# Kernel optimization log

Hardware: AMD Instinct MI355X
Metric: run time of the kernel (lower is better)

## Reference

```python
import jax, jax.numpy as jnp
import numpy as np

B, C_IN, C_MID, C_OUT, R, K = 2048, 64, 64, 128, 60, 13
EPS = 1e-5


def _gather(x, nei):
    # x: [B, C, 60] -> gather neighbors -> [B, C, 60, 13]
    b, c = x.shape[0], x.shape[1]
    return x[:, :, nei].reshape(b, c, R, K)


def _block(x, nei, g, bta, m, v, W, c):
    # BN (eval mode) -> ReLU -> Conv2d(kernel (1,13)) fused block.
    h = _gather(x, nei)                              # [B,C,60,13]
    inv = g * jax.lax.rsqrt(v + EPS)                 # [C]
    h = jax.nn.relu(h * inv[None, :, None, None] + (bta - m * inv)[None, :, None, None])
    # Conv2d with kernel (1,13), stride 1 == contraction over (c, k)
    return jnp.einsum('bcrk,ock->bor', h, W) + c[None, :, None]  # [B,O,60]


def setup_inputs() -> dict:
    key = jax.random.key(0)
    ks = jax.random.split(key, 24)
    n = lambda k, s: jax.random.normal(k, s, dtype=jnp.float32)
    u = lambda k, s: jax.random.uniform(k, s, dtype=jnp.float32, minval=0.5, maxval=1.5)
    return {
        "x": n(ks[0], (B, C_IN, R)),
        "nei": jax.random.randint(ks[1], (R * K,), 0, R, dtype=jnp.int32),
        # comb_layer_in: BN(in) + Conv(in->mid)
        "g1": n(ks[2], (C_IN,)), "b1": n(ks[3], (C_IN,)), "m1": n(ks[4], (C_IN,)), "v1": u(ks[5], (C_IN,)),
        "W1": n(ks[6], (C_MID, C_IN, K)) * 0.1, "c1": n(ks[7], (C_MID,)) * 0.1,
        # comb_layer_out: BN(mid) + Conv(mid->out)
        "g2": n(ks[8], (C_MID,)), "b2": n(ks[9], (C_MID,)), "m2": n(ks[10], (C_MID,)), "v2": u(ks[11], (C_MID,)),
        "W2": n(ks[12], (C_OUT, C_MID, K)) * 0.1, "c2": n(ks[13], (C_OUT,)) * 0.1,
        # short_cut_layer: BN(in) + Conv(in->out)
        "g3": n(ks[14], (C_IN,)), "b3": n(ks[15], (C_IN,)), "m3": n(ks[16], (C_IN,)), "v3": u(ks[17], (C_IN,)),
        "W3": n(ks[18], (C_OUT, C_IN, K)) * 0.1, "c3": n(ks[19], (C_OUT,)) * 0.1,
    }


def reference(x, nei, g1, b1, m1, v1, W1, c1, g2, b2, m2, v2, W2, c2,
              g3, b3, m3, v3, W3, c3):
    f = _block(x, nei, g1, b1, m1, v1, W1, c1)      # [B, C_MID, 60]
    f = _block(f, nei, g2, b2, m2, v2, W2, c2)      # [B, C_OUT, 60]
    sc = _block(x, nei, g3, b3, m3, v3, W3, c3)     # [B, C_OUT, 60]
    return f + sc
```

## Files before the change

kernel.cpp:

```cpp
#include <hip/hip_runtime.h>
#include <hip/hip_bf16.h>


typedef __attribute__((ext_vector_type(8))) short bf16x8;
typedef __attribute__((ext_vector_type(4))) float f32x4;
typedef __attribute__((ext_vector_type(4))) unsigned short us4;
typedef __attribute__((ext_vector_type(8))) unsigned short us8;

#define EPSV 1e-5f
#define PLANE 131072
#define ZTOT  7864320

__device__ __forceinline__ unsigned short f2bf(float f) {
  unsigned int u = __builtin_bit_cast(unsigned int, f);
  u += 0x7FFFu + ((u >> 16) & 1u);
  return (unsigned short)(u >> 16);
}
__device__ __forceinline__ float bf2f(unsigned short s) {
  unsigned int u = ((unsigned int)s) << 16;
  return __builtin_bit_cast(float, u);
}

typedef const __attribute__((address_space(1))) unsigned int gas_u32;
typedef __attribute__((address_space(3))) unsigned int las_u32;
__device__ __forceinline__ void gl16(const void* g, void* l) {
  __builtin_amdgcn_global_load_lds((gas_u32*)g, (las_u32*)l, 16, 0, 0);
}

__global__ void prep_w(const float* __restrict__ W1, const float* __restrict__ W2,
                       const float* __restrict__ W3,
                       const float* __restrict__ g1, const float* __restrict__ be1,
                       const float* __restrict__ mu1, const float* __restrict__ va1,
                       const float* __restrict__ c1,
                       const float* __restrict__ g2, const float* __restrict__ be2,
                       const float* __restrict__ mu2, const float* __restrict__ va2,
                       const float* __restrict__ c2,
                       const float* __restrict__ g3, const float* __restrict__ be3,
                       const float* __restrict__ mu3, const float* __restrict__ va3,
                       const float* __restrict__ c3,
                       unsigned short* __restrict__ W1t,
                       unsigned short* __restrict__ W23t,
                       float* __restrict__ params) {
  int t = blockIdx.x * 256 + threadIdx.x;
  if (t < 4096) {
    int o = t >> 6, c = t & 63;
    const float* src = W1 + (o * 64 + c) * 13;
    unsigned short* dst = W1t + o * 832 + c;
    #pragma unroll
    for (int ks = 0; ks < 13; ks++) dst[ks * 64] = f2bf(src[ks]);
  } else if (t < 20480) {
    int idx = t - 4096;
    int half = idx >> 13;
    int o = (idx >> 6) & 127, c = idx & 63;
    const float* src = (half ? W3 : W2) + (o * 64 + c) * 13;
    unsigned short* dst = W23t + o * 1664 + half * 13 * 64 + c;
    #pragma unroll
    for (int ks = 0; ks < 13; ks++) dst[ks * 64] = f2bf(src[ks]);
  }
  if (blockIdx.x == 79) {
    int u = threadIdx.x;
    if (u < 64) {
      float a1v = g1[u] * rsqrtf(va1[u] + EPSV);
      params[u]       = a1v;
      params[64 + u]  = be1[u] - mu1[u] * a1v;
      float a3v = g3[u] * rsqrtf(va3[u] + EPSV);
      params[128 + u] = a3v;
      params[192 + u] = be3[u] - mu3[u] * a3v;
      float a2v = g2[u] * rsqrtf(va2[u] + EPSV);
      params[256 + u] = a2v;
      params[320 + u] = be2[u] - mu2[u] * a2v + a2v * c1[u];
    }
    if (u < 128) params[384 + u] = c2[u] + c3[u];
  }
}

__global__ __launch_bounds__(256) void t_in(const float* __restrict__ x,
                                            const float* __restrict__ params,
                                            unsigned short* __restrict__ z1T,
                                            unsigned short* __restrict__ z3T) {
  __shared__ float xt[64 * 61];
  __shared__ float prm[256];
  const int b = blockIdx.x, t = threadIdx.x;
  prm[t] = params[t];
  for (int i = t; i < 3840; i += 256) {
    int c = i / 60;
    xt[c * 61 + (i - c * 60)] = x[b * 3840 + i];
  }
  __syncthreads();
  if (t < 240) {
    int r = t >> 2, g = t & 3, c0 = g << 4;
    us8 z1v0, z1v1, z3v0, z3v1;
    #pragma unroll
    for (int j = 0; j < 8; j++) {
      int c = c0 + j;
      float v = xt[c * 61 + r];
      z1v0[j] = f2bf(fmaxf(fmaf(v, prm[c], prm[64 + c]), 0.f));
      z3v0[j] = f2bf(fmaxf(fmaf(v, prm[128 + c], prm[192 + c]), 0.f));
    }
    #pragma unroll
    for (int j = 0; j < 8; j++) {
      int c = c0 + 8 + j;
      float v = xt[c * 61 + r];
      z1v1[j] = f2bf(fmaxf(fmaf(v, prm[c], prm[64 + c]), 0.f));
      z3v1[j] = f2bf(fmaxf(fmaf(v, prm[128 + c], prm[192 + c]), 0.f));
    }
    int idx = (r * 2048 + b) * 64 + c0;
    *(us8*)(z1T + idx) = z1v0;  *(us8*)(z1T + idx + 8) = z1v1;
    *(us8*)(z3T + idx) = z3v0;  *(us8*)(z3T + idx + 8) = z3v1;
  }
}

#define MFMA __builtin_amdgcn_mfma_f32_16x16x32_bf16

__global__ __launch_bounds__(256, 2) void gemm1(const unsigned short* __restrict__ W1t,
                                                const unsigned short* __restrict__ z1T,
                                                const int* __restrict__ nei,
                                                const float* __restrict__ params,
                                                unsigned short* __restrict__ z2T) {
  __shared__ unsigned short As[3][2048];
  __shared__ unsigned short Bs[3][8192];
  __shared__ int sOff[13];

  const int bid = blockIdx.x;
  const int r = bid >> 3, btile = bid & 7;
  const int b0 = btile << 8;
  const int t = threadIdx.x, wv = t >> 6, lane = t & 63;
  const int quad = lane >> 4, nl = lane & 15;

  if (t < 13) sOff[t] = nei[r * 13 + t] * (PLANE * 2);

  const int lr = lane >> 2, lj = lane & 3;
  const int sj = ((lj ^ ((lr >> 1) & 3)) << 4);
  const int aoff = (16 * wv + lr) * 1664 + sj;
  int boff[4];
  #pragma unroll
  for (int i = 0; i < 4; i++) boff[i] = (b0 + 16 * (4 * wv + i) + lr) * 128 + sj;

  const char* gAb = (const char*)W1t;
  const char* z1b = (const char*)z1T;

  __syncthreads();

  {
    const char* gb = z1b + sOff[0];
    gl16(gAb + aoff, &As[0][wv * 512]);
    #pragma unroll
    for (int i = 0; i < 4; i++) gl16(gb + boff[i], &Bs[0][(4 * wv + i) * 512]);
    gl16(gAb + 64 + aoff, &As[1][wv * 512]);
    #pragma unroll
    for (int i = 0; i < 4; i++) gl16(gb + 64 + boff[i], &Bs[1][(4 * wv + i) * 512]);
  }
  asm volatile("s_waitcnt vmcnt(5)" ::: "memory");
  __builtin_amdgcn_s_barrier();

  const int rc = ((quad ^ ((nl >> 1) & 3)) << 3);
  const int aro = nl * 32 + rc;
  const int bro = (wv * 64 + nl) * 32 + rc;

  f32x4 acc[4][4] = {};
  int cb = 0, sb = 2;
  #pragma unroll 1
  for (int s = 0; s < 25; s++) {
    const unsigned short* Ab = &As[cb][aro];
    const unsigned short* Bb = &Bs[cb][bro];
    bf16x8 af[4], bfr[4];
    #pragma unroll
    for (int mt = 0; mt < 4; mt++)
      af[mt] = *(const bf16x8*)(Ab + mt * 512);
    #pragma unroll
    for (int nt = 0; nt < 4; nt++)
      bfr[nt] = *(const bf16x8*)(Bb + nt * 512);
    const int kn = s + 2;
    if (kn < 26) {
      const int pn = kn >> 1;
      int off = sOff[pn] + ((kn & 1) << 6);
      const char* ga = gAb + kn * 64;
      const char* gb = z1b + off;
      gl16(ga + aoff, &As[sb][wv * 512]);
      #pragma unroll
      for (int i = 0; i < 4; i++) gl16(gb + boff[i], &Bs[sb][(4 * wv + i) * 512]);
    }
    __builtin_amdgcn_s_barrier();
    asm volatile("s_waitcnt lgkmcnt(0)" ::: "memory");
    __builtin_amdgcn_sched_barrier(0);
    __builtin_amdgcn_s_setprio(1);
    #pragma unroll
    for (int mt = 0; mt < 4; mt++)
      #pragma unroll
      for (int nt = 0; nt < 4; nt++)
        acc[mt][nt] = MFMA(af[mt], bfr[nt], acc[mt][nt], 0, 0, 0);
    __builtin_amdgcn_s_setprio(0);
    __builtin_amdgcn_sched_barrier(0);
    asm volatile("s_waitcnt vmcnt(5)" ::: "memory");
    __builtin_amdgcn_s_barrier();
    cb = (cb == 2) ? 0 : cb + 1;
    sb = (sb == 2) ? 0 : sb + 1;
  }
  {
    asm volatile("s_waitcnt vmcnt(0)" ::: "memory");
    __builtin_amdgcn_s_barrier();
    const unsigned short* Ab = &As[1][aro];
    const unsigned short* Bb = &Bs[1][bro];
    bf16x8 af[4], bfr[4];
    #pragma unroll
    for (int mt = 0; mt < 4; mt++)
      af[mt] = *(const bf16x8*)(Ab + mt * 512);
    #pragma unroll
    for (int nt = 0; nt < 4; nt++)
      bfr[nt] = *(const bf16x8*)(Bb + nt * 512);
    #pragma unroll
    for (int mt = 0; mt < 4; mt++)
      #pragma unroll
      for (int nt = 0; nt < 4; nt++)
        acc[mt][nt] = MFMA(af[mt], bfr[nt], acc[mt][nt], 0, 0, 0);
  }

  #pragma unroll
  for (int mt = 0; mt < 4; mt++) {
    int ob = mt * 16 + quad * 4;
    f32x4 av = *(const f32x4*)(params + 256 + ob);
    f32x4 bv = *(const f32x4*)(params + 320 + ob);
    #pragma unroll
    for (int nt = 0; nt < 4; nt++) {
      int col = b0 + wv * 64 + nt * 16 + nl;
      f32x4 a = acc[mt][nt];
      us4 w;
      w.x = f2bf(fmaxf(fmaf(a[0], av[0], bv[0]), 0.f));
      w.y = f2bf(fmaxf(fmaf(a[1], av[1], bv[1]), 0.f));
      w.z = f2bf(fmaxf(fmaf(a[2], av[2], bv[2]), 0.f));
      w.w = f2bf(fmaxf(fmaf(a[3], av[3], bv[3]), 0.f));
      *(us4*)(z2T + (r * 2048 + col) * 64 + ob) = w;
    }
  }
}

__global__ __launch_bounds__(256, 2) void gemm2(const unsigned short* __restrict__ W23t,
                                                const unsigned short* __restrict__ z2T,
                                                const unsigned short* __restrict__ z3T,
                                                const int* __restrict__ nei,
                                                const float* __restrict__ params,
                                                unsigned short* __restrict__ outT) {
  __shared__ unsigned short As[3][4096];
  __shared__ unsigned short Bs[3][8192];
  __shared__ int sOff[26];

  const int bid = blockIdx.x;
  const int r = bid >> 3, btile = bid & 7;
  const int b0 = btile << 8;
  const int t = threadIdx.x, wv = t >> 6, lane = t & 63;
  const int quad = lane >> 4, nl = lane & 15;
  const int mh = wv >> 1, nh = wv & 1;

  if (t < 26) {
    int idx = t < 13 ? t : t - 13;
    int p = nei[r * 13 + idx];
    sOff[t] = p * (PLANE * 2) + (t < 13 ? 0 : ZTOT * 2);
  }

  const int lr = lane >> 2, lj = lane & 3;
  const int sj = ((lj ^ ((lr >> 1) & 3)) << 4);
  int aoff[2];
  #pragma unroll
  for (int i = 0; i < 2; i++) aoff[i] = (16 * (2 * wv + i) + lr) * 3328 + sj;
  int boff[4];
  #pragma unroll
  for (int i = 0; i < 4; i++) boff[i] = (b0 + 16 * (4 * wv + i) + lr) * 128 + sj;

  const char* gAb = (const char*)W23t;
  const char* z2b = (const char*)z2T;

  __syncthreads();

  {
    const char* gb = z2b + sOff[0];
    #pragma unroll
    for (int i = 0; i < 2; i++) gl16(gAb + aoff[i], &As[0][(2 * wv + i) * 512]);
    #pragma unroll
    for (int i = 0; i < 4; i++) gl16(gb + boff[i], &Bs[0][(4 * wv + i) * 512]);
    #pragma unroll
    for (int i = 0; i < 2; i++) gl16(gAb + 64 + aoff[i], &As[1][(2 * wv + i) * 512]);
    #pragma unroll
    for (int i = 0; i < 4; i++) gl16(gb + 64 + boff[i], &Bs[1][(4 * wv + i) * 512]);
  }
  asm volatile("s_waitcnt vmcnt(6)" ::: "memory");
  __builtin_amdgcn_s_barrier();

  const int rc = ((quad ^ ((nl >> 1) & 3)) << 3);
  const int aro = (mh * 64 + nl) * 32 + rc;
  const int bro = (nh * 128 + nl) * 32 + rc;

  f32x4 acc[4][8] = {};
  int cb = 0, sb = 2;
  #pragma unroll 1
  for (int s = 0; s < 51; s++) {
    const unsigned short* Ab = &As[cb][aro];
    const unsigned short* Bb = &Bs[cb][bro];
    bf16x8 af[4], bfr[8];
    #pragma unroll
    for (int mt = 0; mt < 4; mt++)
      af[mt] = *(const bf16x8*)(Ab + mt * 512);
    #pragma unroll
    for (int nt = 0; nt < 8; nt++)
      bfr[nt] = *(const bf16x8*)(Bb + nt * 512);
    const int kn = s + 2;
    if (kn < 52) {
      const int pn = kn >> 1;
      int off = sOff[pn] + ((kn & 1) << 6);
      const char* ga = gAb + kn * 64;
      const char* gb = z2b + off;
      #pragma unroll
      for (int i = 0; i < 2; i++) gl16(ga + aoff[i], &As[sb][(2 * wv + i) * 512]);
      #pragma unroll
      for (int i = 0; i < 4; i++) gl16(gb + boff[i], &Bs[sb][(4 * wv + i) * 512]);
    }
    __builtin_amdgcn_s_barrier();
    asm volatile("s_waitcnt lgkmcnt(0)" ::: "memory");
    __builtin_amdgcn_sched_barrier(0);
    __builtin_amdgcn_s_setprio(1);
    #pragma unroll
    for (int mt = 0; mt < 4; mt++)
      #pragma unroll
      for (int nt = 0; nt < 8; nt++)
        acc[mt][nt] = MFMA(af[mt], bfr[nt], acc[mt][nt], 0, 0, 0);
    __builtin_amdgcn_s_setprio(0);
    __builtin_amdgcn_sched_barrier(0);
    asm volatile("s_waitcnt vmcnt(6)" ::: "memory");
    __builtin_amdgcn_s_barrier();
    cb = (cb == 2) ? 0 : cb + 1;
    sb = (sb == 2) ? 0 : sb + 1;
  }
  {
    asm volatile("s_waitcnt vmcnt(0)" ::: "memory");
    __builtin_amdgcn_s_barrier();
    const unsigned short* Ab = &As[0][aro];
    const unsigned short* Bb = &Bs[0][bro];
    bf16x8 af[4], bfr[8];
    #pragma unroll
    for (int mt = 0; mt < 4; mt++)
      af[mt] = *(const bf16x8*)(Ab + mt * 512);
    #pragma unroll
    for (int nt = 0; nt < 8; nt++)
      bfr[nt] = *(const bf16x8*)(Bb + nt * 512);
    #pragma unroll
    for (int mt = 0; mt < 4; mt++)
      #pragma unroll
      for (int nt = 0; nt < 8; nt++)
        acc[mt][nt] = MFMA(af[mt], bfr[nt], acc[mt][nt], 0, 0, 0);
  }

  #pragma unroll
  for (int mt = 0; mt < 4; mt++) {
    int ob = mh * 64 + mt * 16 + quad * 4;
    f32x4 cv = *(const f32x4*)(params + 384 + ob);
    #pragma unroll
    for (int nt = 0; nt < 8; nt++) {
      int col = b0 + nh * 128 + nt * 16 + nl;
      f32x4 a = acc[mt][nt];
      us4 w;
      w.x = f2bf(a[0] + cv[0]);
      w.y = f2bf(a[1] + cv[1]);
      w.z = f2bf(a[2] + cv[2]);
      w.w = f2bf(a[3] + cv[3]);
      *(us4*)(outT + (r * 2048 + col) * 128 + ob) = w;
    }
  }
}

__global__ __launch_bounds__(256) void t_out(const unsigned short* __restrict__ outT,
                                             float* __restrict__ out) {
  __shared__ float ot[60 * 129];
  const int b = blockIdx.x, t = threadIdx.x;
  for (int i = t; i < 1920; i += 256) {
    int r = i >> 5, og = (i & 31) << 2;
    us4 v = *(const us4*)(outT + (r * 2048 + b) * 128 + og);
    ot[r * 129 + og + 0] = bf2f(v.x);
    ot[r * 129 + og + 1] = bf2f(v.y);
    ot[r * 129 + og + 2] = bf2f(v.z);
    ot[r * 129 + og + 3] = bf2f(v.w);
  }
  __syncthreads();
  float* dst = out + b * 7680;
  for (int i = t; i < 7680; i += 256) {
    int o = i / 60, r = i - o * 60;
    dst[i] = ot[r * 129 + o];
  }
}

extern "C" void kernel_launch(void* const* d_in, const int* in_sizes, int n_in,
                              void* d_out, int out_size, void* d_ws, size_t ws_size,
                              hipStream_t stream) {
  const float* x   = (const float*)d_in[0];
  const int*   nei = (const int*)d_in[1];
  const float* g1  = (const float*)d_in[2];
  const float* be1 = (const float*)d_in[3];
  const float* mu1 = (const float*)d_in[4];
  const float* va1 = (const float*)d_in[5];
  const float* W1  = (const float*)d_in[6];
  const float* c1  = (const float*)d_in[7];
  const float* g2  = (const float*)d_in[8];
  const float* be2 = (const float*)d_in[9];
  const float* mu2 = (const float*)d_in[10];
  const float* va2 = (const float*)d_in[11];
  const float* W2  = (const float*)d_in[12];
  const float* c2  = (const float*)d_in[13];
  const float* g3  = (const float*)d_in[14];
  const float* be3 = (const float*)d_in[15];
  const float* mu3 = (const float*)d_in[16];
  const float* va3 = (const float*)d_in[17];
  const float* W3  = (const float*)d_in[18];
  const float* c3  = (const float*)d_in[19];

  unsigned short* W1t  = (unsigned short*)d_ws;
  unsigned short* W23t = W1t + 53248;
  float*          prm  = (float*)(W23t + 212992);
  unsigned short* z2T  = (unsigned short*)(prm + 512);
  unsigned short* z3T  = z2T + ZTOT;
  unsigned short* big  = z3T + ZTOT;
  unsigned short* z1T  = big;
  unsigned short* outT = big;

  prep_w<<<80, 256, 0, stream>>>(W1, W2, W3,
                                 g1, be1, mu1, va1, c1,
                                 g2, be2, mu2, va2, c2,
                                 g3, be3, mu3, va3, c3,
                                 W1t, W23t, prm);
  t_in<<<2048, 256, 0, stream>>>(x, prm, z1T, z3T);
  gemm1<<<480, 256, 0, stream>>>(W1t, z1T, nei, prm, z2T);
  gemm2<<<480, 256, 0, stream>>>(W23t, z2T, z3T, nei, prm, outT);
  t_out<<<2048, 256, 0, stream>>>(outT, (float*)d_out);
}
```

Measured before the change: 224.2 us.

## Load weight fragments directly from global into registers, drop LDS staging for A

Both GEMM kernels stop staging the weight (A) operand through shared memory. Each lane now loads its MFMA A-fragments straight from global memory, prefetching one step ahead into registers (afN to afC), while the gathered activations keep the LDS triple-buffer. The goal is to cut LDS traffic and footprint and the async-copy instructions for A. The cost is extra per-lane global loads, relying on cache hits for the shared weights, and more VGPR pressure. The tail prefetch is clamped to avoid branching, and the vmcnt waits are retuned to match.

```diff
diff --git a/kernel.cpp b/kernel.cpp
--- a/kernel.cpp
+++ b/kernel.cpp
@@ -117,7 +117,6 @@
                                                 const int* __restrict__ nei,
                                                 const float* __restrict__ params,
                                                 unsigned short* __restrict__ z2T) {
-  __shared__ unsigned short As[3][2048];
   __shared__ unsigned short Bs[3][8192];
   __shared__ int sOff[13];
 
@@ -131,52 +130,54 @@
 
   const int lr = lane >> 2, lj = lane & 3;
   const int sj = ((lj ^ ((lr >> 1) & 3)) << 4);
-  const int aoff = (16 * wv + lr) * 1664 + sj;
   int boff[4];
   #pragma unroll
   for (int i = 0; i < 4; i++) boff[i] = (b0 + 16 * (4 * wv + i) + lr) * 128 + sj;
 
-  const char* gAb = (const char*)W1t;
+  const unsigned short* gA = W1t + nl * 832 + quad * 8;
+
   const char* z1b = (const char*)z1T;
 
   __syncthreads();
 
+  bf16x8 afC[4], afN[4];
+  #pragma unroll
+  for (int mt = 0; mt < 4; mt++)
+    afC[mt] = *(const bf16x8*)(gA + mt * 13312);
   {
     const char* gb = z1b + sOff[0];
-    gl16(gAb + aoff, &As[0][wv * 512]);
     #pragma unroll
     for (int i = 0; i < 4; i++) gl16(gb + boff[i], &Bs[0][(4 * wv + i) * 512]);
-    gl16(gAb + 64 + aoff, &As[1][wv * 512]);
     #pragma unroll
     for (int i = 0; i < 4; i++) gl16(gb + 64 + boff[i], &Bs[1][(4 * wv + i) * 512]);
   }
-  asm volatile("s_waitcnt vmcnt(5)" ::: "memory");
+  asm volatile("s_waitcnt vmcnt(0)" ::: "memory");
   __builtin_amdgcn_s_barrier();
 
   const int rc = ((quad ^ ((nl >> 1) & 3)) << 3);
-  const int aro = nl * 32 + rc;
   const int bro = (wv * 64 + nl) * 32 + rc;
 
   f32x4 acc[4][4] = {};
   int cb = 0, sb = 2;
   #pragma unroll 1
   for (int s = 0; s < 25; s++) {
-    const unsigned short* Ab = &As[cb][aro];
+    {
+      const unsigned short* ga = gA + (s + 1) * 32;
+      #pragma unroll
+      for (int mt = 0; mt < 4; mt++)
+        afN[mt] = *(const bf16x8*)(ga + mt * 13312);
+    }
+    __builtin_amdgcn_sched_barrier(0);
     const unsigned short* Bb = &Bs[cb][bro];
-    bf16x8 af[4], bfr[4];
-    #pragma unroll
-    for (int mt = 0; mt < 4; mt++)
-      af[mt] = *(const bf16x8*)(Ab + mt * 512);
+    bf16x8 bfr[4];
     #pragma unroll
     for (int nt = 0; nt < 4; nt++)
       bfr[nt] = *(const bf16x8*)(Bb + nt * 512);
-    const int kn = s + 2;
-    if (kn < 26) {
-      const int pn = kn >> 1;
+    {
+      const int kn = s + 2;
+      int pn = kn >> 1; if (pn > 12) pn = 12;
       int off = sOff[pn] + ((kn & 1) << 6);
-      const char* ga = gAb + kn * 64;
       const char* gb = z1b + off;
-      gl16(ga + aoff, &As[sb][wv * 512]);
       #pragma unroll
       for (int i = 0; i < 4; i++) gl16(gb + boff[i], &Bs[sb][(4 * wv + i) * 512]);
     }
@@ -188,31 +189,30 @@
     for (int mt = 0; mt < 4; mt++)
       #pragma unroll
       for (int nt = 0; nt < 4; nt++)
-        acc[mt][nt] = MFMA(af[mt], bfr[nt], acc[mt][nt], 0, 0, 0);
+        acc[mt][nt] = MFMA(afC[mt], bfr[nt], acc[mt][nt], 0, 0, 0);
     __builtin_amdgcn_s_setprio(0);
     __builtin_amdgcn_sched_barrier(0);
-    asm volatile("s_waitcnt vmcnt(5)" ::: "memory");
+    #pragma unroll
+    for (int mt = 0; mt < 4; mt++) afC[mt] = afN[mt];
+    __builtin_amdgcn_sched_barrier(0);
+    asm volatile("s_waitcnt vmcnt(8)" ::: "memory");
     __builtin_amdgcn_s_barrier();
     cb = (cb == 2) ? 0 : cb + 1;
     sb = (sb == 2) ? 0 : sb + 1;
   }
   {
-    asm volatile("s_waitcnt vmcnt(0)" ::: "memory");
-    __builtin_amdgcn_s_barrier();
-    const unsigned short* Ab = &As[1][aro];
     const unsigned short* Bb = &Bs[1][bro];
-    bf16x8 af[4], bfr[4];
-    #pragma unroll
-    for (int mt = 0; mt < 4; mt++)
-      af[mt] = *(const bf16x8*)(Ab + mt * 512);
+    bf16x8 bfr[4];
     #pragma unroll
     for (int nt = 0; nt < 4; nt++)
       bfr[nt] = *(const bf16x8*)(Bb + nt * 512);
+    asm volatile("s_waitcnt lgkmcnt(0)" ::: "memory");
+    __builtin_amdgcn_sched_barrier(0);
     #pragma unroll
     for (int mt = 0; mt < 4; mt++)
       #pragma unroll
       for (int nt = 0; nt < 4; nt++)
-        acc[mt][nt] = MFMA(af[mt], bfr[nt], acc[mt][nt], 0, 0, 0);
+        acc[mt][nt] = MFMA(afC[mt], bfr[nt], acc[mt][nt], 0, 0, 0);
   }
 
   #pragma unroll
@@ -240,7 +240,6 @@
                                                 const int* __restrict__ nei,
                                                 const float* __restrict__ params,
                                                 unsigned short* __restrict__ outT) {
-  __shared__ unsigned short As[3][4096];
   __shared__ unsigned short Bs[3][8192];
   __shared__ int sOff[26];
 
@@ -259,57 +258,54 @@
 
   const int lr = lane >> 2, lj = lane & 3;
   const int sj = ((lj ^ ((lr >> 1) & 3)) << 4);
-  int aoff[2];
-  #pragma unroll
-  for (int i = 0; i < 2; i++) aoff[i] = (16 * (2 * wv + i) + lr) * 3328 + sj;
   int boff[4];
   #pragma unroll
   for (int i = 0; i < 4; i++) boff[i] = (b0 + 16 * (4 * wv + i) + lr) * 128 + sj;
 
-  const char* gAb = (const char*)W23t;
+  const unsigned short* gA = W23t + (mh * 64 + nl) * 1664 + quad * 8;
+
   const char* z2b = (const char*)z2T;
 
   __syncthreads();
 
+  bf16x8 afC[4], afN[4];
+  #pragma unroll
+  for (int mt = 0; mt < 4; mt++)
+    afC[mt] = *(const bf16x8*)(gA + mt * 26624);
   {
     const char* gb = z2b + sOff[0];
     #pragma unroll
-    for (int i = 0; i < 2; i++) gl16(gAb + aoff[i], &As[0][(2 * wv + i) * 512]);
-    #pragma unroll
     for (int i = 0; i < 4; i++) gl16(gb + boff[i], &Bs[0][(4 * wv + i) * 512]);
     #pragma unroll
-    for (int i = 0; i < 2; i++) gl16(gAb + 64 + aoff[i], &As[1][(2 * wv + i) * 512]);
-    #pragma unroll
     for (int i = 0; i < 4; i++) gl16(gb + 64 + boff[i], &Bs[1][(4 * wv + i) * 512]);
   }
-  asm volatile("s_waitcnt vmcnt(6)" ::: "memory");
+  asm volatile("s_waitcnt vmcnt(0)" ::: "memory");
   __builtin_amdgcn_s_barrier();
 
   const int rc = ((quad ^ ((nl >> 1) & 3)) << 3);
-  const int aro = (mh * 64 + nl) * 32 + rc;
   const int bro = (nh * 128 + nl) * 32 + rc;
 
   f32x4 acc[4][8] = {};
   int cb = 0, sb = 2;
   #pragma unroll 1
   for (int s = 0; s < 51; s++) {
-    const unsigned short* Ab = &As[cb][aro];
+    {
+      const unsigned short* ga = gA + (s + 1) * 32;
+      #pragma unroll
+      for (int mt = 0; mt < 4; mt++)
+        afN[mt] = *(const bf16x8*)(ga + mt * 26624);
+    }
+    __builtin_amdgcn_sched_barrier(0);
     const unsigned short* Bb = &Bs[cb][bro];
-    bf16x8 af[4], bfr[8];
-    #pragma unroll
-    for (int mt = 0; mt < 4; mt++)
-      af[mt] = *(const bf16x8*)(Ab + mt * 512);
+    bf16x8 bfr[8];
     #pragma unroll
     for (int nt = 0; nt < 8; nt++)
       bfr[nt] = *(const bf16x8*)(Bb + nt * 512);
-    const int kn = s + 2;
-    if (kn < 52) {
-      const int pn = kn >> 1;
+    {
+      const int kn = s + 2;
+      int pn = kn >> 1; if (pn > 25) pn = 25;
       int off = sOff[pn] + ((kn & 1) << 6);
-      const char* ga = gAb + kn * 64;
       const char* gb = z2b + off;
-      #pragma unroll
-      for (int i = 0; i < 2; i++) gl16(ga + aoff[i], &As[sb][(2 * wv + i) * 512]);
       #pragma unroll
       for (int i = 0; i < 4; i++) gl16(gb + boff[i], &Bs[sb][(4 * wv + i) * 512]);
     }
@@ -321,31 +317,30 @@
     for (int mt = 0; mt < 4; mt++)
       #pragma unroll
       for (int nt = 0; nt < 8; nt++)
-        acc[mt][nt] = MFMA(af[mt], bfr[nt], acc[mt][nt], 0, 0, 0);
+        acc[mt][nt] = MFMA(afC[mt], bfr[nt], acc[mt][nt], 0, 0, 0);
     __builtin_amdgcn_s_setprio(0);
     __builtin_amdgcn_sched_barrier(0);
-    asm volatile("s_waitcnt vmcnt(6)" ::: "memory");
+    #pragma unroll
+    for (int mt = 0; mt < 4; mt++) afC[mt] = afN[mt];
+    __builtin_amdgcn_sched_barrier(0);
+    asm volatile("s_waitcnt vmcnt(8)" ::: "memory");
     __builtin_amdgcn_s_barrier();
     cb = (cb == 2) ? 0 : cb + 1;
     sb = (sb == 2) ? 0 : sb + 1;
   }
   {
-    asm volatile("s_waitcnt vmcnt(0)" ::: "memory");
-    __builtin_amdgcn_s_barrier();
-    const unsigned short* Ab = &As[0][aro];
     const unsigned short* Bb = &Bs[0][bro];
-    bf16x8 af[4], bfr[8];
-    #pragma unroll
-    for (int mt = 0; mt < 4; mt++)
-      af[mt] = *(const bf16x8*)(Ab + mt * 512);
+    bf16x8 bfr[8];
     #pragma unroll
     for (int nt = 0; nt < 8; nt++)
       bfr[nt] = *(const bf16x8*)(Bb + nt * 512);
+    asm volatile("s_waitcnt lgkmcnt(0)" ::: "memory");
+    __builtin_amdgcn_sched_barrier(0);
     #pragma unroll
     for (int mt = 0; mt < 4; mt++)
       #pragma unroll
       for (int nt = 0; nt < 8; nt++)
-        acc[mt][nt] = MFMA(af[mt], bfr[nt], acc[mt][nt], 0, 0, 0);
+        acc[mt][nt] = MFMA(afC[mt], bfr[nt], acc[mt][nt], 0, 0, 0);
   }
 
   #pragma unroll
```

Result: slower. 256.3 us (+14.3%).
